# Kernel tuning notes

Hardware: AMD Instinct MI355X
Metric: run time of the kernel (lower is better)

## Reference

```python
import jax, jax.numpy as jnp
import numpy as np

B, S, D = 256, 256, 1024
P = D // 2  # proj_dim default = input_dim / 2
NUM_HIDDEN = 2
EPS = 1e-7  # K.epsilon()
INIT_SCALE = 0.05  # keras 'uniform' init


def setup_inputs() -> dict:
    key = jax.random.key(0)
    ks = jax.random.split(key, 8)
    x = jax.random.normal(ks[0], (B, S, D), dtype=jnp.float32)
    mask = jax.random.randint(ks[1], (B, S), 0, 2).astype(bool)
    u = lambda k, shp: jax.random.uniform(k, shp, jnp.float32, -INIT_SCALE, INIT_SCALE)
    proj_head = u(ks[2], (D, P))
    proj_prep = u(ks[3], (D, P))
    proj_child = u(ks[4], (D, P))
    hidden_layers = u(ks[5], (NUM_HIDDEN, P, P))
    scorer = u(ks[6], (P,))
    return {"x": x, "proj_head": proj_head, "proj_prep": proj_prep,
            "proj_child": proj_child, "hidden_layers": hidden_layers,
            "scorer": scorer, "mask": mask}


def reference(x, proj_head, proj_prep, proj_child, hidden_layers, scorer, mask):
    # x: [B, S, D]; last two timesteps are preposition and child noun.
    head_enc = x[:, :-2, :]          # [B, S-2, D]
    prep_enc = x[:, -2, :]           # [B, D]
    child_enc = x[:, -1, :]          # [B, D]

    head_proj = jnp.einsum('bsd,dp->bsp', head_enc, proj_head)      # [B, S-2, P]
    prep_proj = (prep_enc @ proj_prep)[:, None, :]                  # [B, 1, P]
    child_proj = (child_enc @ proj_child)[:, None, :]               # [B, 1, P]

    # composition_type == 'HPCT'
    composed = jnp.tanh(head_proj + prep_proj + child_proj)         # [B, S-2, P]

    for i in range(hidden_layers.shape[0]):  # small fixed layer count
        composed = jnp.tanh(jnp.einsum('bsp,pq->bsq', composed, hidden_layers[i]))

    scores = jnp.einsum('bsp,p->bs', composed, scorer)              # [B, S-2]

    # masked exp-normalization (as in the original Keras code)
    exp_scores = jnp.exp(scores)
    head_mask = mask[:, :-2]
    masked_exp = jnp.where(head_mask, exp_scores, 0.0)
    exp_sum = jnp.sum(masked_exp, axis=1, keepdims=True) + EPS
    return masked_exp / exp_sum
```

## Files before the change

kernel.cpp:

```cpp
#include <hip/hip_runtime.h>
#include <hip/hip_bf16.h>
#include <stdint.h>

#define B_ 256
#define S_ 256
#define D_ 1024
#define P_ 512
#define SH 254
#define M_ (B_*SH)
#define EPSF 1e-7f

typedef __attribute__((ext_vector_type(8))) short short8v;
typedef __attribute__((ext_vector_type(4))) short short4v;
typedef __attribute__((ext_vector_type(4))) float float4v;

__device__ inline short f2bf(float f) {
  __hip_bfloat16 h = __float2bfloat16(f);
  return *reinterpret_cast<short*>(&h);
}
__device__ inline float bf2f(short u) {
  union { float f; unsigned int i; } c;
  c.i = ((unsigned int)(unsigned short)u) << 16;
  return c.f;
}
__device__ inline float fast_tanh(float x) {
  float e = __expf(2.0f * x);
  return 1.0f - 2.0f * __builtin_amdgcn_rcpf(e + 1.0f);
}

__global__ void k_detect(const unsigned char* m, int* flag) {
  __shared__ int c0, c3;
  if (threadIdx.x == 0) { c0 = 0; c3 = 0; }
  __syncthreads();
  int f0 = 0, f3 = 0;
  for (int i = threadIdx.x; i < 4096; i += 256) {
    unsigned char v = m[i];
    if (v != 0) {
      if ((i & 3) == 0) f0 = 1;
      if ((i & 3) == 3) f3 = 1;
    }
  }
  if (f0) atomicOr(&c0, 1);
  if (f3) atomicOr(&c3, 1);
  __syncthreads();
  if (threadIdx.x == 0) {
    int f;
    if (c3 == 0) f = 0;
    else if (c0 != 0) f = 1;
    else f = 2;
    *flag = f;
  }
}

__global__ void k_conv_pcw(const float* wp, const float* wc, short* op, short* oc) {
  int idx = blockIdx.x * 256 + threadIdx.x;
  if (idx < D_*P_) op[idx] = f2bf(wp[idx]);
  else { int j = idx - D_*P_; oc[j] = f2bf(wc[j]); }
}

__global__ void k_trans_head(const float* w, short* out) {
  int idx = blockIdx.x * 256 + threadIdx.x;
  int n = idx & (P_ - 1);
  int k = idx >> 9;
  out[(k >> 5) * (P_*32) + n*32 + (k & 31)] = f2bf(w[k*P_ + n]);
}

__global__ void k_trans_hidden(const float* h, short* o0, short* o1) {
  int idx = blockIdx.x * 256 + threadIdx.x;
  int which = idx >> 18;
  int j = idx & ((P_*P_) - 1);
  int n = j & (P_ - 1);
  int k = j >> 9;
  short v = f2bf(h[which*(P_*P_) + k*P_ + n]);
  short* o = which ? o1 : o0;
  o[(k >> 5) * (P_*32) + n*32 + (k & 31)] = v;
}

__global__ void __launch_bounds__(256) k_pc(const float* __restrict__ x,
                                            const short* __restrict__ wp,
                                            const short* __restrict__ wc,
                                            float* __restrict__ pc) {
  __shared__ float xp[D_], xc[D_];
  int b = blockIdx.x, t = threadIdx.x;
  const float* xb = x + ((size_t)b * S_ + SH) * D_;
  for (int i = t; i < D_; i += 256) { xp[i] = xb[i]; xc[i] = xb[D_ + i]; }
  __syncthreads();
  float a0 = 0.f, a1 = 0.f;
  int p0 = t, p1 = t + 256;
  for (int d = 0; d < D_; d++) {
    float vp = xp[d], vc = xc[d];
    a0 += vp * bf2f(wp[d*P_ + p0]) + vc * bf2f(wc[d*P_ + p0]);
    a1 += vp * bf2f(wp[d*P_ + p1]) + vc * bf2f(wc[d*P_ + p1]);
  }
  pc[b*P_ + p0] = a0;
  pc[b*P_ + p1] = a1;
}

__global__ void __launch_bounds__(512, 2) k_main(
    const float* __restrict__ x, const short* __restrict__ wth,
    const short* __restrict__ h0t, const short* __restrict__ h1t,
    const float* __restrict__ scorer, const float* __restrict__ pc,
    float* __restrict__ scores)
{
  __shared__ __attribute__((aligned(16))) short As[64*40];
  __shared__ __attribute__((aligned(16))) short Bs[512*40];
  __shared__ __attribute__((aligned(16))) short Cs[64*520];
  __shared__ float scorer_s[P_];
  __shared__ float score_s[64];

  const int tid  = threadIdx.x;
  const int lane = tid & 63;
  const int w    = tid >> 6;
  const int wm   = w & 1, wn = w >> 1;
  const int l15  = lane & 15, quad = lane >> 4;
  const int rowbase = blockIdx.x * 64;

  if (tid < P_) scorer_s[tid] = scorer[tid];

  const int arow = tid >> 3;
  const int acol = (tid & 7) * 4;
  {
  }
  int r0 = rowbase + arow;
  int ab = r0 / SH;
  int as_ = r0 - ab * SH;
  const float* aptr = x + ((size_t)(ab * S_ + as_)) * D_ + acol;

  float4v acc[2][8];
  #pragma unroll
  for (int i = 0; i < 2; i++)
    #pragma unroll
    for (int j = 0; j < 8; j++) acc[i][j] = (float4v){0.f,0.f,0.f,0.f};

  for (int kc = 0; kc < 32; kc++) {
    {
      float4 v = *(const float4*)(aptr + kc*32);
      short4v sv = { f2bf(v.x), f2bf(v.y), f2bf(v.z), f2bf(v.w) };
      *(short4v*)&As[arow*40 + (tid & 7)*4] = sv;
    }
    {
      const uint4* src = (const uint4*)(wth + kc*(P_*32));
      #pragma unroll
      for (int i = 0; i < 4; i++) {
        int c = tid + i*512;
        uint4 v = src[c];
        int n = c >> 2, un = c & 3;
        *(uint4*)&Bs[n*40 + un*8] = v;
      }
    }
    __syncthreads();
    short8v a0 = *(const short8v*)&As[(wm*32 +      l15)*40 + quad*8];
    short8v a1 = *(const short8v*)&As[(wm*32 + 16 + l15)*40 + quad*8];
    #pragma unroll
    for (int nt = 0; nt < 8; nt++) {
      short8v bfr = *(const short8v*)&Bs[(wn*128 + nt*16 + l15)*40 + quad*8];
      acc[0][nt] = __builtin_amdgcn_mfma_f32_16x16x32_bf16(a0, bfr, acc[0][nt], 0, 0, 0);
      acc[1][nt] = __builtin_amdgcn_mfma_f32_16x16x32_bf16(a1, bfr, acc[1][nt], 0, 0, 0);
    }
    __syncthreads();
  }

  #pragma unroll
  for (int mt = 0; mt < 2; mt++) {
    #pragma unroll
    for (int j = 0; j < 4; j++) {
      int rl = wm*32 + mt*16 + quad*4 + j;
      int rg = rowbase + rl;
      int bb = rg / SH;
      const float* pcb = pc + bb*P_;
      #pragma unroll
      for (int nt = 0; nt < 8; nt++) {
        int col = wn*128 + nt*16 + l15;
        float v = fast_tanh(acc[mt][nt][j] + pcb[col]);
        Cs[rl*520 + col] = f2bf(v);
      }
    }
  }
  __syncthreads();

  for (int stage = 0; stage < 2; stage++) {
    const short* ht = stage ? h1t : h0t;
    #pragma unroll
    for (int i = 0; i < 2; i++)
      #pragma unroll
      for (int j = 0; j < 8; j++) acc[i][j] = (float4v){0.f,0.f,0.f,0.f};
    for (int kc = 0; kc < 16; kc++) {
      const uint4* src = (const uint4*)(ht + kc*(P_*32));
      #pragma unroll
      for (int i = 0; i < 4; i++) {
        int c = tid + i*512;
        uint4 v = src[c];
        int n = c >> 2, un = c & 3;
        *(uint4*)&Bs[n*40 + un*8] = v;
      }
      __syncthreads();
      short8v a0 = *(const short8v*)&Cs[(wm*32 +      l15)*520 + kc*32 + quad*8];
      short8v a1 = *(const short8v*)&Cs[(wm*32 + 16 + l15)*520 + kc*32 + quad*8];
      #pragma unroll
      for (int nt = 0; nt < 8; nt++) {
        short8v bfr = *(const short8v*)&Bs[(wn*128 + nt*16 + l15)*40 + quad*8];
        acc[0][nt] = __builtin_amdgcn_mfma_f32_16x16x32_bf16(a0, bfr, acc[0][nt], 0, 0, 0);
        acc[1][nt] = __builtin_amdgcn_mfma_f32_16x16x32_bf16(a1, bfr, acc[1][nt], 0, 0, 0);
      }
      __syncthreads();
    }
    if (stage == 0) {
      #pragma unroll
      for (int mt = 0; mt < 2; mt++) {
        #pragma unroll
        for (int j = 0; j < 4; j++) {
          int rl = wm*32 + mt*16 + quad*4 + j;
          #pragma unroll
          for (int nt = 0; nt < 8; nt++) {
            int col = wn*128 + nt*16 + l15;
            Cs[rl*520 + col] = f2bf(fast_tanh(acc[mt][nt][j]));
          }
        }
      }
      __syncthreads();
    }
  }

  if (tid < 64) score_s[tid] = 0.f;
  __syncthreads();
  #pragma unroll
  for (int mt = 0; mt < 2; mt++) {
    #pragma unroll
    for (int j = 0; j < 4; j++) {
      float part = 0.f;
      #pragma unroll
      for (int nt = 0; nt < 8; nt++) {
        int col = wn*128 + nt*16 + l15;
        part += fast_tanh(acc[mt][nt][j]) * scorer_s[col];
      }
      #pragma unroll
      for (int o = 1; o < 16; o <<= 1) part += __shfl_xor(part, o, 64);
      if (l15 == 0) atomicAdd(&score_s[wm*32 + mt*16 + quad*4 + j], part);
    }
  }
  __syncthreads();
  if (tid < 64) scores[rowbase + tid] = __expf(score_s[tid]);
}

__global__ void __launch_bounds__(256) k_softmax(const float* __restrict__ scores,
                                                 const void* __restrict__ mask,
                                                 const int* __restrict__ flag,
                                                 float* __restrict__ out) {
  int b = blockIdx.x, t = threadIdx.x;
  int lane = t & 63, w = t >> 6;
  __shared__ float ps[4];
  float me = 0.f;
  bool valid = t < SH;
  if (valid) {
    float e = scores[b*SH + t];
    int f = *flag;
    bool mb;
    if (f == 1)      mb = ((const unsigned char*)mask)[b*S_ + t] != 0;
    else if (f == 2) mb = ((const float*)mask)[b*S_ + t] != 0.0f;
    else             mb = ((const int*)mask)[b*S_ + t] != 0;
    me = mb ? e : 0.f;
  }
  float v = me;
  for (int o = 1; o < 64; o <<= 1) v += __shfl_xor(v, o, 64);
  if (lane == 0) ps[w] = v;
  __syncthreads();
  float tot = ps[0] + ps[1] + ps[2] + ps[3] + EPSF;
  if (valid) out[b*SH + t] = me / tot;
}

extern "C" void kernel_launch(void* const* d_in, const int* in_sizes, int n_in,
                              void* d_out, int out_size, void* d_ws, size_t ws_size,
                              hipStream_t stream) {
  const float* x          = (const float*)d_in[0];
  const float* proj_head  = (const float*)d_in[1];
  const float* proj_prep  = (const float*)d_in[2];
  const float* proj_child = (const float*)d_in[3];
  const float* hidden     = (const float*)d_in[4];
  const float* scorer     = (const float*)d_in[5];
  const void*  mask       = d_in[6];
  float* out = (float*)d_out;
  char* ws = (char*)d_ws;

  int*   flag   = (int*)  (ws + 0);
  float* pc     = (float*)(ws + 256);
  short* wth    = (short*)(ws + 524544);
  short* h0t    = (short*)(ws + 1573120);
  short* h1t    = (short*)(ws + 2097408);
  short* wpb    = (short*)(ws + 2621696);
  short* wcb    = (short*)(ws + 3670272);
  float* scores = (float*)(ws + 4718848);

  k_detect<<<1, 256, 0, stream>>>((const unsigned char*)mask, flag);
  k_conv_pcw<<<4096, 256, 0, stream>>>(proj_prep, proj_child, wpb, wcb);
  k_trans_head<<<2048, 256, 0, stream>>>(proj_head, wth);
  k_trans_hidden<<<2048, 256, 0, stream>>>(hidden, h0t, h1t);
  k_pc<<<256, 256, 0, stream>>>(x, wpb, wcb, pc);
  k_main<<<1016, 512, 0, stream>>>(x, wth, h0t, h1t, scorer, pc, scores);
  k_softmax<<<256, 256, 0, stream>>>(scores, mask, flag, out);
}
```

Before: 744.8 us.

## Restructure main GEMM to read B from global, double-buffer A, rework pc kernel

The main fused MLP kernel drops the shared-memory staging of weight tiles. Each wave now owns a 64-column slice across all 64 rows and reads its B fragments straight from global/L2, which removes most of the per-k-step barriers. The A tile is loaded in 128-wide K chunks and double-buffered with register prefetch. Epilogue stores are packed into 32-bit writes. The prep/child projection kernel reads the fp32 weights directly, tiled over 16 batches with shared x, so the bf16 conversion kernel goes away; the cost is more global/L2 traffic for B fragments.

```diff
diff --git a/kernel.cpp b/kernel.cpp
--- a/kernel.cpp
+++ b/kernel.cpp
@@ -11,17 +11,11 @@
 #define EPSF 1e-7f
 
 typedef __attribute__((ext_vector_type(8))) short short8v;
-typedef __attribute__((ext_vector_type(4))) short short4v;
 typedef __attribute__((ext_vector_type(4))) float float4v;
 
 __device__ inline short f2bf(float f) {
   __hip_bfloat16 h = __float2bfloat16(f);
   return *reinterpret_cast<short*>(&h);
-}
-__device__ inline float bf2f(short u) {
-  union { float f; unsigned int i; } c;
-  c.i = ((unsigned int)(unsigned short)u) << 16;
-  return c.f;
 }
 __device__ inline float fast_tanh(float x) {
   float e = __expf(2.0f * x);
@@ -52,12 +46,6 @@
   }
 }
 
-__global__ void k_conv_pcw(const float* wp, const float* wc, short* op, short* oc) {
-  int idx = blockIdx.x * 256 + threadIdx.x;
-  if (idx < D_*P_) op[idx] = f2bf(wp[idx]);
-  else { int j = idx - D_*P_; oc[j] = f2bf(wc[j]); }
-}
-
 __global__ void k_trans_head(const float* w, short* out) {
   int idx = blockIdx.x * 256 + threadIdx.x;
   int n = idx & (P_ - 1);
@@ -76,24 +64,36 @@
   o[(k >> 5) * (P_*32) + n*32 + (k & 31)] = v;
 }
 
-__global__ void __launch_bounds__(256) k_pc(const float* __restrict__ x,
-                                            const short* __restrict__ wp,
-                                            const short* __restrict__ wc,
+__global__ void __launch_bounds__(512) k_pc(const float* __restrict__ x,
+                                            const float* __restrict__ wp,
+                                            const float* __restrict__ wc,
                                             float* __restrict__ pc) {
-  __shared__ float xp[D_], xc[D_];
-  int b = blockIdx.x, t = threadIdx.x;
-  const float* xb = x + ((size_t)b * S_ + SH) * D_;
-  for (int i = t; i < D_; i += 256) { xp[i] = xb[i]; xc[i] = xb[D_ + i]; }
-  __syncthreads();
-  float a0 = 0.f, a1 = 0.f;
-  int p0 = t, p1 = t + 256;
-  for (int d = 0; d < D_; d++) {
-    float vp = xp[d], vc = xc[d];
-    a0 += vp * bf2f(wp[d*P_ + p0]) + vc * bf2f(wc[d*P_ + p0]);
-    a1 += vp * bf2f(wp[d*P_ + p1]) + vc * bf2f(wc[d*P_ + p1]);
-  }
-  pc[b*P_ + p0] = a0;
-  pc[b*P_ + p1] = a1;
+  __shared__ float xs[16][256];
+  int bg = blockIdx.x >> 4, cs = blockIdx.x & 15;
+  int t = threadIdx.x;
+  int bloc = t >> 5, c = t & 31;
+  int batch = bg * 16 + bloc;
+  int col = cs * 32 + c;
+  float acc = 0.f;
+  #pragma unroll
+  for (int half = 0; half < 2; half++) {
+    const float* wsrc = half ? wc : wp;
+    for (int kc = 0; kc < 4; kc++) {
+      const float* xr = x + ((size_t)(batch * S_ + SH + half)) * D_ + kc*256 + c*8;
+      float4 v0 = *(const float4*)(xr + 0);
+      float4 v1 = *(const float4*)(xr + 4);
+      __syncthreads();
+      *(float4*)&xs[bloc][c*8 + 0] = v0;
+      *(float4*)&xs[bloc][c*8 + 4] = v1;
+      __syncthreads();
+      const float* wv = wsrc + (size_t)(kc*256) * P_ + col;
+      #pragma unroll 8
+      for (int d = 0; d < 256; d++) {
+        acc += xs[bloc][d] * wv[(size_t)d * P_];
+      }
+    }
+  }
+  pc[batch * P_ + col] = acc;
 }
 
 __global__ void __launch_bounds__(512, 2) k_main(
@@ -102,140 +102,166 @@
     const float* __restrict__ scorer, const float* __restrict__ pc,
     float* __restrict__ scores)
 {
-  __shared__ __attribute__((aligned(16))) short As[64*40];
-  __shared__ __attribute__((aligned(16))) short Bs[512*40];
+  __shared__ __attribute__((aligned(16))) short As[2][64*136];
   __shared__ __attribute__((aligned(16))) short Cs[64*520];
   __shared__ float scorer_s[P_];
   __shared__ float score_s[64];
 
   const int tid  = threadIdx.x;
   const int lane = tid & 63;
-  const int w    = tid >> 6;
-  const int wm   = w & 1, wn = w >> 1;
+  const int wn   = tid >> 6;
   const int l15  = lane & 15, quad = lane >> 4;
   const int rowbase = blockIdx.x * 64;
 
-  if (tid < P_) scorer_s[tid] = scorer[tid];
+  scorer_s[tid] = scorer[tid];
+  if (tid < 64) score_s[tid] = 0.f;
 
   const int arow = tid >> 3;
-  const int acol = (tid & 7) * 4;
+  const int akg  = (tid & 7) * 16;
   {
-  }
-  int r0 = rowbase + arow;
-  int ab = r0 / SH;
-  int as_ = r0 - ab * SH;
-  const float* aptr = x + ((size_t)(ab * S_ + as_)) * D_ + acol;
-
-  float4v acc[2][8];
-  #pragma unroll
-  for (int i = 0; i < 2; i++)
+    int r0 = rowbase + arow;
+    int ab = r0 / SH;
+    int as_ = r0 - ab * SH;
+    const float* aptr = x + ((size_t)(ab * S_ + as_)) * D_ + akg;
+
+    float4 st0 = *(const float4*)(aptr + 0);
+    float4 st1 = *(const float4*)(aptr + 4);
+    float4 st2 = *(const float4*)(aptr + 8);
+    float4 st3 = *(const float4*)(aptr + 12);
+    short8v s0 = { f2bf(st0.x),f2bf(st0.y),f2bf(st0.z),f2bf(st0.w),
+                   f2bf(st1.x),f2bf(st1.y),f2bf(st1.z),f2bf(st1.w) };
+    short8v s1 = { f2bf(st2.x),f2bf(st2.y),f2bf(st2.z),f2bf(st2.w),
+                   f2bf(st3.x),f2bf(st3.y),f2bf(st3.z),f2bf(st3.w) };
+    *(short8v*)&As[0][arow*136 + akg]     = s0;
+    *(short8v*)&As[0][arow*136 + akg + 8] = s1;
+    __syncthreads();
+
+    float4v acc[4][4];
     #pragma unroll
-    for (int j = 0; j < 8; j++) acc[i][j] = (float4v){0.f,0.f,0.f,0.f};
-
-  for (int kc = 0; kc < 32; kc++) {
-    {
-      float4 v = *(const float4*)(aptr + kc*32);
-      short4v sv = { f2bf(v.x), f2bf(v.y), f2bf(v.z), f2bf(v.w) };
-      *(short4v*)&As[arow*40 + (tid & 7)*4] = sv;
-    }
-    {
-      const uint4* src = (const uint4*)(wth + kc*(P_*32));
-      #pragma unroll
-      for (int i = 0; i < 4; i++) {
-        int c = tid + i*512;
-        uint4 v = src[c];
-        int n = c >> 2, un = c & 3;
-        *(uint4*)&Bs[n*40 + un*8] = v;
+    for (int i = 0; i < 4; i++)
+      #pragma unroll
+      for (int j = 0; j < 4; j++) acc[i][j] = (float4v){0.f,0.f,0.f,0.f};
+
+    const uint4* wb = (const uint4*)wth;
+
+    for (int sc = 0; sc < 8; sc++) {
+      const int cur = sc & 1;
+      float4 n0, n1, n2, n3;
+      if (sc < 7) {
+        const float* p = aptr + (sc + 1) * 128;
+        n0 = *(const float4*)(p + 0);
+        n1 = *(const float4*)(p + 4);
+        n2 = *(const float4*)(p + 8);
+        n3 = *(const float4*)(p + 12);
+      }
+      #pragma unroll
+      for (int c = 0; c < 4; c++) {
+        const int kc = sc * 4 + c;
+        short8v a[4];
+        #pragma unroll
+        for (int mt = 0; mt < 4; mt++)
+          a[mt] = *(const short8v*)&As[cur][(mt*16 + l15)*136 + c*32 + quad*8];
+        #pragma unroll
+        for (int nt = 0; nt < 4; nt++) {
+          uint4 bv = wb[(size_t)kc*2048 + (wn*64 + nt*16 + l15)*4 + quad];
+          short8v bfr = *(short8v*)&bv;
+          #pragma unroll
+          for (int mt = 0; mt < 4; mt++)
+            acc[mt][nt] = __builtin_amdgcn_mfma_f32_16x16x32_bf16(a[mt], bfr, acc[mt][nt], 0, 0, 0);
+        }
+      }
+      if (sc < 7) {
+        short8v w0 = { f2bf(n0.x),f2bf(n0.y),f2bf(n0.z),f2bf(n0.w),
+                       f2bf(n1.x),f2bf(n1.y),f2bf(n1.z),f2bf(n1.w) };
+        short8v w1 = { f2bf(n2.x),f2bf(n2.y),f2bf(n2.z),f2bf(n2.w),
+                       f2bf(n3.x),f2bf(n3.y),f2bf(n3.z),f2bf(n3.w) };
+        *(short8v*)&As[cur ^ 1][arow*136 + akg]     = w0;
+        *(short8v*)&As[cur ^ 1][arow*136 + akg + 8] = w1;
+      }
+      __syncthreads();
+    }
+
+    #pragma unroll
+    for (int mt = 0; mt < 4; mt++) {
+      #pragma unroll
+      for (int j = 0; j < 4; j++) {
+        int rl = mt*16 + quad*4 + j;
+        int rg = rowbase + rl;
+        int bb = rg / SH;
+        const float* pcb = pc + bb * P_;
+        #pragma unroll
+        for (int nt = 0; nt < 4; nt++) {
+          int col = wn*64 + nt*16 + l15;
+          float v = fast_tanh(acc[mt][nt][j] + pcb[col]);
+          float o = __shfl_xor(v, 1, 64);
+          unsigned hs = (unsigned short)f2bf(v);
+          unsigned ho = (unsigned short)f2bf(o);
+          if ((l15 & 1) == 0)
+            *(unsigned*)&Cs[rl*520 + col] = hs | (ho << 16);
+        }
       }
     }
     __syncthreads();
-    short8v a0 = *(const short8v*)&As[(wm*32 +      l15)*40 + quad*8];
-    short8v a1 = *(const short8v*)&As[(wm*32 + 16 + l15)*40 + quad*8];
+
+    #pragma unroll 1
+    for (int stage = 0; stage < 2; stage++) {
+      const uint4* hb = (const uint4*)(stage ? h1t : h0t);
+      #pragma unroll
+      for (int i = 0; i < 4; i++)
+        #pragma unroll
+        for (int j = 0; j < 4; j++) acc[i][j] = (float4v){0.f,0.f,0.f,0.f};
+      #pragma unroll 4
+      for (int kc = 0; kc < 16; kc++) {
+        short8v a[4];
+        #pragma unroll
+        for (int mt = 0; mt < 4; mt++)
+          a[mt] = *(const short8v*)&Cs[(mt*16 + l15)*520 + kc*32 + quad*8];
+        #pragma unroll
+        for (int nt = 0; nt < 4; nt++) {
+          uint4 bv = hb[(size_t)kc*2048 + (wn*64 + nt*16 + l15)*4 + quad];
+          short8v bfr = *(short8v*)&bv;
+          #pragma unroll
+          for (int mt = 0; mt < 4; mt++)
+            acc[mt][nt] = __builtin_amdgcn_mfma_f32_16x16x32_bf16(a[mt], bfr, acc[mt][nt], 0, 0, 0);
+        }
+      }
+      if (stage == 0) {
+        __syncthreads();
+        #pragma unroll
+        for (int mt = 0; mt < 4; mt++) {
+          #pragma unroll
+          for (int j = 0; j < 4; j++) {
+            int rl = mt*16 + quad*4 + j;
+            #pragma unroll
+            for (int nt = 0; nt < 4; nt++) {
+              int col = wn*64 + nt*16 + l15;
+              float v = fast_tanh(acc[mt][nt][j]);
+              float o = __shfl_xor(v, 1, 64);
+              unsigned hs = (unsigned short)f2bf(v);
+              unsigned ho = (unsigned short)f2bf(o);
+              if ((l15 & 1) == 0)
+                *(unsigned*)&Cs[rl*520 + col] = hs | (ho << 16);
+            }
+          }
+        }
+        __syncthreads();
+      }
+    }
+
     #pragma unroll
-    for (int nt = 0; nt < 8; nt++) {
-      short8v bfr = *(const short8v*)&Bs[(wn*128 + nt*16 + l15)*40 + quad*8];
-      acc[0][nt] = __builtin_amdgcn_mfma_f32_16x16x32_bf16(a0, bfr, acc[0][nt], 0, 0, 0);
-      acc[1][nt] = __builtin_amdgcn_mfma_f32_16x16x32_bf16(a1, bfr, acc[1][nt], 0, 0, 0);
-    }
-    __syncthreads();
-  }
-
-  #pragma unroll
-  for (int mt = 0; mt < 2; mt++) {
-    #pragma unroll
-    for (int j = 0; j < 4; j++) {
-      int rl = wm*32 + mt*16 + quad*4 + j;
-      int rg = rowbase + rl;
-      int bb = rg / SH;
-      const float* pcb = pc + bb*P_;
-      #pragma unroll
-      for (int nt = 0; nt < 8; nt++) {
-        int col = wn*128 + nt*16 + l15;
-        float v = fast_tanh(acc[mt][nt][j] + pcb[col]);
-        Cs[rl*520 + col] = f2bf(v);
-      }
-    }
-  }
-  __syncthreads();
-
-  for (int stage = 0; stage < 2; stage++) {
-    const short* ht = stage ? h1t : h0t;
-    #pragma unroll
-    for (int i = 0; i < 2; i++)
-      #pragma unroll
-      for (int j = 0; j < 8; j++) acc[i][j] = (float4v){0.f,0.f,0.f,0.f};
-    for (int kc = 0; kc < 16; kc++) {
-      const uint4* src = (const uint4*)(ht + kc*(P_*32));
-      #pragma unroll
-      for (int i = 0; i < 4; i++) {
-        int c = tid + i*512;
-        uint4 v = src[c];
-        int n = c >> 2, un = c & 3;
-        *(uint4*)&Bs[n*40 + un*8] = v;
-      }
-      __syncthreads();
-      short8v a0 = *(const short8v*)&Cs[(wm*32 +      l15)*520 + kc*32 + quad*8];
-      short8v a1 = *(const short8v*)&Cs[(wm*32 + 16 + l15)*520 + kc*32 + quad*8];
-      #pragma unroll
-      for (int nt = 0; nt < 8; nt++) {
-        short8v bfr = *(const short8v*)&Bs[(wn*128 + nt*16 + l15)*40 + quad*8];
-        acc[0][nt] = __builtin_amdgcn_mfma_f32_16x16x32_bf16(a0, bfr, acc[0][nt], 0, 0, 0);
-        acc[1][nt] = __builtin_amdgcn_mfma_f32_16x16x32_bf16(a1, bfr, acc[1][nt], 0, 0, 0);
-      }
-      __syncthreads();
-    }
-    if (stage == 0) {
-      #pragma unroll
-      for (int mt = 0; mt < 2; mt++) {
-        #pragma unroll
-        for (int j = 0; j < 4; j++) {
-          int rl = wm*32 + mt*16 + quad*4 + j;
-          #pragma unroll
-          for (int nt = 0; nt < 8; nt++) {
-            int col = wn*128 + nt*16 + l15;
-            Cs[rl*520 + col] = f2bf(fast_tanh(acc[mt][nt][j]));
-          }
-        }
-      }
-      __syncthreads();
-    }
-  }
-
-  if (tid < 64) score_s[tid] = 0.f;
-  __syncthreads();
-  #pragma unroll
-  for (int mt = 0; mt < 2; mt++) {
-    #pragma unroll
-    for (int j = 0; j < 4; j++) {
-      float part = 0.f;
-      #pragma unroll
-      for (int nt = 0; nt < 8; nt++) {
-        int col = wn*128 + nt*16 + l15;
-        part += fast_tanh(acc[mt][nt][j]) * scorer_s[col];
-      }
-      #pragma unroll
-      for (int o = 1; o < 16; o <<= 1) part += __shfl_xor(part, o, 64);
-      if (l15 == 0) atomicAdd(&score_s[wm*32 + mt*16 + quad*4 + j], part);
+    for (int mt = 0; mt < 4; mt++) {
+      #pragma unroll
+      for (int j = 0; j < 4; j++) {
+        float part = 0.f;
+        #pragma unroll
+        for (int nt = 0; nt < 4; nt++) {
+          int col = wn*64 + nt*16 + l15;
+          part += fast_tanh(acc[mt][nt][j]) * scorer_s[col];
+        }
+        #pragma unroll
+        for (int o = 1; o < 16; o <<= 1) part += __shfl_xor(part, o, 64);
+        if (l15 == 0) atomicAdd(&score_s[mt*16 + quad*4 + j], part);
+      }
     }
   }
   __syncthreads();
@@ -286,15 +312,12 @@
   short* wth    = (short*)(ws + 524544);
   short* h0t    = (short*)(ws + 1573120);
   short* h1t    = (short*)(ws + 2097408);
-  short* wpb    = (short*)(ws + 2621696);
-  short* wcb    = (short*)(ws + 3670272);
-  float* scores = (float*)(ws + 4718848);
+  float* scores = (float*)(ws + 2621696);
 
   k_detect<<<1, 256, 0, stream>>>((const unsigned char*)mask, flag);
-  k_conv_pcw<<<4096, 256, 0, stream>>>(proj_prep, proj_child, wpb, wcb);
   k_trans_head<<<2048, 256, 0, stream>>>(proj_head, wth);
   k_trans_hidden<<<2048, 256, 0, stream>>>(hidden, h0t, h1t);
-  k_pc<<<256, 256, 0, stream>>>(x, wpb, wcb, pc);
+  k_pc<<<256, 512, 0, stream>>>(x, proj_prep, proj_child, pc);
   k_main<<<1016, 512, 0, stream>>>(x, wth, h0t, h1t, scorer, pc, scores);
   k_softmax<<<256, 256, 0, stream>>>(scores, mask, flag, out);
 }
```

Measured after the change: 745.5 us. About the same (+0.1%).
